# Kernel optimization log

Hardware: AMD Instinct MI355X
Metric: run time of the kernel (lower is better)

Reference implementation:

```python
import jax, jax.numpy as jnp
import numpy as np

NEG_SLOPE = 0.2


def _gat_layer(x, edge_index, W, a_src, a_dst, b):
    """PyG GATConv: linear -> per-edge attention logits -> segment softmax over
    destination -> scatter-add weighted messages. Self-loops added (PyG default)."""
    N = x.shape[0]
    heads, out = a_src.shape
    loops = jnp.arange(N, dtype=edge_index.dtype)
    src = jnp.concatenate([edge_index[0], loops])
    dst = jnp.concatenate([edge_index[1], loops])
    xh = (x @ W).reshape(N, heads, out)                      # [N,H,D]
    alpha_s = (xh * a_src).sum(-1)                           # [N,H]
    alpha_d = (xh * a_dst).sum(-1)                           # [N,H]
    e = jax.nn.leaky_relu(alpha_s[src] + alpha_d[dst], NEG_SLOPE)  # [E,H]
    emax = jax.ops.segment_max(e, dst, num_segments=N)       # [N,H]
    ex = jnp.exp(e - emax[dst])
    den = jax.ops.segment_sum(ex, dst, num_segments=N)
    att = ex / (den[dst] + 1e-16)                            # [E,H]
    msg = xh[src] * att[..., None]                           # [E,H,D]
    o = jax.ops.segment_sum(msg, dst, num_segments=N)        # [N,H,D]
    return o.reshape(N, heads * out) + b


def _single_source_gnn(h, edge_index, params):
    n_layers = len(params)
    for i, (W, a_s, a_d, b) in enumerate(params):
        h = _gat_layer(h, edge_index, W, a_s, a_d, b)
        if i < n_layers - 1:
            h = jax.nn.relu(h)
    return h


def setup_inputs() -> dict:
    key = jax.random.key(0)
    B, N, H, heads, deg = 4, 2000, 64, 4, 32
    E = N * deg
    ks = jax.random.split(key, 20)

    def mk_edge_index(k):
        e = jax.random.randint(k, (2, B, E), 0, N)
        off = (jnp.arange(B) * N)[None, :, None]
        return (e + off).reshape(2, B * E).astype(jnp.int32)

    inp = {
        "h0_flat": jax.random.normal(ks[0], (B * N, H), jnp.float32),
        "edge_index_s1": mk_edge_index(ks[1]),
        "edge_index_s2": mk_edge_index(ks[2]),
    }
    dims = [(H, H * heads), (H * heads, H * heads)]
    i = 3
    for s in ("s1", "s2"):
        for l, (din, dout) in enumerate(dims):
            inp[f"W_{s}_{l}"] = jax.random.normal(ks[i], (din, dout), jnp.float32) * 0.1; i += 1
            inp[f"a_src_{s}_{l}"] = jax.random.normal(ks[i], (heads, H), jnp.float32) * 0.1; i += 1
            inp[f"a_dst_{s}_{l}"] = jax.random.normal(ks[i], (heads, H), jnp.float32) * 0.1; i += 1
            inp[f"b_{s}_{l}"] = jnp.zeros((dout,), jnp.float32)
    inp["batch_size"] = B
    inp["num_stocks"] = N
    return inp


def reference(h0_flat, edge_index_s1, edge_index_s2,
              W_s1_0, a_src_s1_0, a_dst_s1_0, b_s1_0,
              W_s1_1, a_src_s1_1, a_dst_s1_1, b_s1_1,
              W_s2_0, a_src_s2_0, a_dst_s2_0, b_s2_0,
              W_s2_1, a_src_s2_1, a_dst_s2_1, b_s2_1,
              batch_size, num_stocks):
    p1 = [(W_s1_0, a_src_s1_0, a_dst_s1_0, b_s1_0),
          (W_s1_1, a_src_s1_1, a_dst_s1_1, b_s1_1)]
    p2 = [(W_s2_0, a_src_s2_0, a_dst_s2_0, b_s2_0),
          (W_s2_1, a_src_s2_1, a_dst_s2_1, b_s2_1)]
    h1 = _single_source_gnn(h0_flat, edge_index_s1, p1)
    h2 = _single_source_gnn(h0_flat, edge_index_s2, p2)
    # dict of per-source outputs in torch -> stacked [n_sources, B*N, H*heads]
    return jnp.stack([h1, h2])
```

## Files before the change

### kernel.cpp

```cpp
#include <hip/hip_runtime.h>
#include <hip/hip_fp16.h>


#define NEG_SLOPE 0.2f
#define ELLW 96
#define EPT 8

typedef _Float16 half8 __attribute__((ext_vector_type(8)));
typedef float floatx4 __attribute__((ext_vector_type(4)));

struct Args {
    const float* h0;
    const int *ei1, *ei2;
    const float *W10, *W11, *W20, *W21;
    const float *as10, *ad10, *b10, *as11, *ad11, *b11;
    const float *as20, *ad20, *b20, *as21, *ad21, *b21;
    _Float16 *Wt10, *Wt20, *Wt11, *Wt21;
    float *vaS1, *vaD1, *vaS2, *vaD2;
    _Float16 *h0h;
    int *cnt, *slots;
    _Float16 *agg1, *agg2;
    _Float16 *xh1, *xh2;
    float *alS1, *alD1, *alS2, *alD2;
    float *out0, *out1;
    int N, E1, E2, AB;
};


__global__ __launch_bounds__(64) void prep_kernel(Args a) {
    int z = blockIdx.z, y = blockIdx.y, c = blockIdx.x;
    int t = threadIdx.x;
    int flat = ((z * gridDim.y + y) * gridDim.x + c) * 64 + t;
    int GT = gridDim.x * gridDim.y * gridDim.z * 64;
    if (flat < 2 * a.N) a.cnt[flat] = 0;
    for (int i = flat; i < a.N * 64; i += GT)
        a.h0h[i] = (_Float16)a.h0[i];
    if (y == 0) {
        const float* W  = z ? a.W20  : a.W10;
        _Float16*    Wt = z ? a.Wt20 : a.Wt10;
        Wt[(size_t)c * 64 + t] = (_Float16)W[(size_t)t * 256 + c];
        if (c < 8) {
            int h = c & 3, sel = c >> 2;
            const float* av = sel ? (z ? a.ad20 : a.ad10)
                                  : (z ? a.as20 : a.as10);
            float* va = sel ? (z ? a.vaD2 : a.vaD1)
                            : (z ? a.vaS2 : a.vaS1);
            float acc = 0.f;
            for (int cc = 0; cc < 64; cc++)
                acc += W[(size_t)t * 256 + h * 64 + cc] * av[h * 64 + cc];
            va[h * 64 + t] = acc;
        }
    } else {
        int k = (y - 1) * 64 + t;
        const float* W  = z ? a.W21  : a.W11;
        _Float16*    Wt = z ? a.Wt21 : a.Wt11;
        Wt[(size_t)c * 256 + k] = (_Float16)W[(size_t)k * 256 + c];
    }
}


__global__ __launch_bounds__(256) void scat_al0_kernel(Args a) {
    int b = blockIdx.x;
    int tid = threadIdx.x;
    if (b < a.AB) {
        int g = b * 4 + (tid >> 6);
        if (g >= 2 * a.N) return;
        int L = tid & 63;
        int s = (g >= a.N) ? 1 : 0;
        int i = g - s * a.N;
        const float* vaS = s ? a.vaS2 : a.vaS1;
        const float* vaD = s ? a.vaD2 : a.vaD1;
        float* alS = s ? a.alS2 : a.alS1;
        float* alD = s ? a.alD2 : a.alD1;
        float x = a.h0[(size_t)i * 64 + L];
#pragma unroll
        for (int h = 0; h < 4; h++) {
            float sv = x * vaS[h * 64 + L];
            float dv = x * vaD[h * 64 + L];
#pragma unroll
            for (int off = 32; off >= 1; off >>= 1) {
                sv += __shfl_xor(sv, off);
                dv += __shfl_xor(dv, off);
            }
            if (L == 0) {
                alS[i * 4 + h] = sv;
                alD[i * 4 + h] = dv;
            }
        }
    } else {
        int sb = b - a.AB;
        int r = sb & 7;
        int chunk = sb >> 3;
        int cpx = (2 * a.N) >> 3;
        int glo = r * cpx, ghi = glo + cpx;
        int tot1 = a.E1 + a.N;
        int tot = tot1 + a.E2 + a.N;
        int base = chunk * (256 * EPT);
#pragma unroll
        for (int k = 0; k < EPT; k++) {
            int j = base + k * 256 + tid;
            if (j >= tot) break;
            int s, jj; const int* ei; int E;
            if (j < tot1) { s = 0; jj = j;        ei = a.ei1; E = a.E1; }
            else          { s = 1; jj = j - tot1; ei = a.ei2; E = a.E2; }
            int dst = (jj < E) ? ei[E + jj] : (jj - E);
            int gg = s * a.N + dst;
            if (gg < glo || gg >= ghi) continue;
            int src = (jj < E) ? ei[jj] : dst;
            int pos = atomicAdd(&a.cnt[gg], 1);
            if (pos < ELLW) a.slots[(size_t)gg * ELLW + pos] = src;
        }
    }
}


__global__ __launch_bounds__(256) void attn_agg_kernel(Args a) {
    __shared__ float2 pairs[4][8][10];
    int tid = threadIdx.x;
    int h = tid >> 6, L = tid & 63, st = L >> 3, lc = L & 7;
    int b = blockIdx.x;
    int cpx = (2 * a.N) >> 3;
    int g = (b & 7) * cpx + (b >> 3);
    int s = (g >= a.N) ? 1 : 0;
    int dst = g - s * a.N;
    const float* alS = s ? a.alS2 : a.alS1;
    const float* alD = s ? a.alD2 : a.alD1;
    _Float16*    agg = s ? a.agg2 : a.agg1;

    const int* slots = a.slots + (size_t)g * ELLW;
    int pre = slots[L];
    int nd = a.cnt[g];
    if (nd > ELLW) nd = ELLW;
    float ad = alD[dst * 4 + h];
    const char* xb = (const char*)a.h0h + lc * 16;

    float acc[8] = {};
    float pden = 0.f;

    for (int c = 0; c < nd; c += 64) {
        int n = nd - c; if (n > 64) n = 64;
        int off = 0; float p = 0.f;
        if (L < n) {
            int src = (c == 0) ? pre : slots[c + L];
            float t = alS[src * 4 + h] + ad;
            t = (t > 0.f) ? t : NEG_SLOPE * t;
            p = __expf(t);
            off = src * 128;
        }
        pden += p;
        pairs[h][L & 7][L >> 3] = make_float2(__int_as_float(off), p);
        int iters = (n + 7) >> 3;
        for (int ii = 0; ii < iters; ii += 4) {
            float4 twoA = *(const float4*)&pairs[h][st][ii];
            float4 twoB = *(const float4*)&pairs[h][st][ii + 2];
            int   o0 = __float_as_int(twoA.x); float w0 = twoA.y;
            int   o1i = __float_as_int(twoA.z); float w1 = twoA.w;
            int   o2i = __float_as_int(twoB.x); float w2 = twoB.y;
            int   o3i = __float_as_int(twoB.z); float w3 = twoB.w;
            float4 r0 = *(const float4*)(xb + o0);
            float4 r1 = *(const float4*)(xb + o1i);
            float4 r2 = *(const float4*)(xb + o2i);
            float4 r3 = *(const float4*)(xb + o3i);
            const __half2* q0 = (const __half2*)&r0;
            const __half2* q1 = (const __half2*)&r1;
            const __half2* q2 = (const __half2*)&r2;
            const __half2* q3 = (const __half2*)&r3;
#pragma unroll
            for (int k = 0; k < 4; k++) {
                acc[2 * k + 0] += (float)q0[k].x * w0;
                acc[2 * k + 1] += (float)q0[k].y * w0;
                acc[2 * k + 0] += (float)q1[k].x * w1;
                acc[2 * k + 1] += (float)q1[k].y * w1;
                acc[2 * k + 0] += (float)q2[k].x * w2;
                acc[2 * k + 1] += (float)q2[k].y * w2;
                acc[2 * k + 0] += (float)q3[k].x * w3;
                acc[2 * k + 1] += (float)q3[k].y * w3;
            }
        }
    }
#pragma unroll
    for (int k = 0; k < 8; k++) {
        acc[k] += __shfl_xor(acc[k], 8);
        acc[k] += __shfl_xor(acc[k], 16);
        acc[k] += __shfl_xor(acc[k], 32);
    }
#pragma unroll
    for (int o2_ = 32; o2_ >= 1; o2_ >>= 1) pden += __shfl_xor(pden, o2_);

    if (st == 0) {
        float d = 1.0f / (pden + 1e-16f);
        int col = h * 64 + lc * 8;
        half8 ov;
#pragma unroll
        for (int k = 0; k < 8; k++) ov[k] = (_Float16)(acc[k] * d);
        *(half8*)(agg + (size_t)dst * 256 + col) = ov;
    }
}


__global__ __launch_bounds__(256) void fusedgemm_kernel(Args a) {
    __shared__ _Float16 hT[32][264];
    int half_ = (a.N / 32);
    int b = blockIdx.x;
    int s = (b >= half_);
    int bx = b - s * half_;
    int row0 = bx * 32;

    const _Float16* agg = s ? a.agg2 : a.agg1;
    const _Float16* Wt0 = s ? a.Wt20 : a.Wt10;
    const _Float16* Wt1 = s ? a.Wt21 : a.Wt11;
    const float* bias0  = s ? a.b20  : a.b10;
    const float* a_s    = s ? a.as21 : a.as11;
    const float* a_d    = s ? a.ad21 : a.ad11;
    _Float16* xh = s ? a.xh2 : a.xh1;
    float* alS = s ? a.alS2 : a.alS1;
    float* alD = s ? a.alD2 : a.alD1;

    int tid  = threadIdx.x;
    int wave = tid >> 6;
    int lane = tid & 63;
    int lo = lane & 15, hi = lane >> 4;
    int c0 = wave * 64;

    {
        floatx4 acc[2][4] = {};
#pragma unroll
        for (int ks = 0; ks < 2; ks++) {
            half8 af[2], bf[4];
#pragma unroll
            for (int f = 0; f < 2; f++)
                af[f] = *(const half8*)(agg + (size_t)(row0 + f * 16 + lo) * 256
                                        + c0 + ks * 32 + hi * 8);
#pragma unroll
            for (int cf = 0; cf < 4; cf++)
                bf[cf] = *(const half8*)(Wt0 + (size_t)(c0 + cf * 16 + lo) * 64
                                         + ks * 32 + hi * 8);
#pragma unroll
            for (int f = 0; f < 2; f++)
#pragma unroll
                for (int cf = 0; cf < 4; cf++)
                    acc[f][cf] = __builtin_amdgcn_mfma_f32_16x16x32_f16(
                        af[f], bf[cf], acc[f][cf], 0, 0, 0);
        }
        float bb[4];
#pragma unroll
        for (int cf = 0; cf < 4; cf++) bb[cf] = bias0[c0 + cf * 16 + lo];
#pragma unroll
        for (int f = 0; f < 2; f++)
#pragma unroll
            for (int cf = 0; cf < 4; cf++)
#pragma unroll
                for (int r = 0; r < 4; r++) {
                    int row = f * 16 + hi * 4 + r;
                    float v = acc[f][cf][r] + bb[cf];
                    hT[row][c0 + cf * 16 + lo] = (_Float16)fmaxf(v, 0.f);
                }
    }
    __syncthreads();

    floatx4 acc[2][4] = {};
#pragma unroll
    for (int ks = 0; ks < 8; ks++) {
        half8 af[2], bf[4];
#pragma unroll
        for (int f = 0; f < 2; f++)
            af[f] = *(const half8*)&hT[f * 16 + lo][ks * 32 + hi * 8];
#pragma unroll
        for (int cf = 0; cf < 4; cf++)
            bf[cf] = *(const half8*)(Wt1 + (size_t)(c0 + cf * 16 + lo) * 256
                                     + ks * 32 + hi * 8);
#pragma unroll
        for (int f = 0; f < 2; f++)
#pragma unroll
            for (int cf = 0; cf < 4; cf++)
                acc[f][cf] = __builtin_amdgcn_mfma_f32_16x16x32_f16(
                    af[f], bf[cf], acc[f][cf], 0, 0, 0);
    }

    float asw[4], adw[4];
#pragma unroll
    for (int cf = 0; cf < 4; cf++) {
        asw[cf] = a_s[c0 + cf * 16 + lo];
        adw[cf] = a_d[c0 + cf * 16 + lo];
    }
#pragma unroll
    for (int f = 0; f < 2; f++) {
#pragma unroll
        for (int r = 0; r < 4; r++) {
            int row = row0 + f * 16 + hi * 4 + r;
            float v0 = acc[f][0][r], v1 = acc[f][1][r];
            float v2 = acc[f][2][r], v3 = acc[f][3][r];
            _Float16* xrow = &xh[(size_t)row * 256 + c0 + lo];
            xrow[0]  = (_Float16)v0;
            xrow[16] = (_Float16)v1;
            xrow[32] = (_Float16)v2;
            xrow[48] = (_Float16)v3;
            float s1 = v0 * asw[0] + v1 * asw[1] + v2 * asw[2] + v3 * asw[3];
            float s2 = v0 * adw[0] + v1 * adw[1] + v2 * adw[2] + v3 * adw[3];
#pragma unroll
            for (int off = 1; off < 16; off <<= 1) {
                s1 += __shfl_xor(s1, off);
                s2 += __shfl_xor(s2, off);
            }
            if (lo == 0) {
                alS[row * 4 + wave] = s1;
                alD[row * 4 + wave] = s2;
            }
        }
    }
}


__global__ __launch_bounds__(256) void attn1_kernel(Args a) {
    __shared__ float2 pairs[4][8][10];
    int tid = threadIdx.x;
    int h = tid >> 6, L = tid & 63, st = L >> 3, lc = L & 7;
    int b = blockIdx.x;
    int cpx = (2 * a.N) >> 3;
    int g = (b & 7) * cpx + (b >> 3);
    int s = (g >= a.N) ? 1 : 0;
    int dst = g - s * a.N;
    const _Float16* xh = s ? a.xh2  : a.xh1;
    const float* alS   = s ? a.alS2 : a.alS1;
    const float* alD   = s ? a.alD2 : a.alD1;
    const float* bias  = s ? a.b21  : a.b11;
    float* out         = s ? a.out1 : a.out0;

    const int* slots = a.slots + (size_t)g * ELLW;
    int pre = slots[L];
    int nd = a.cnt[g];
    if (nd > ELLW) nd = ELLW;
    float ad = alD[dst * 4 + h];
    const char* xb = (const char*)xh + h * 128 + lc * 16;

    float acc[8] = {};
    float pden = 0.f;

    for (int c = 0; c < nd; c += 64) {
        int n = nd - c; if (n > 64) n = 64;
        int off = 0; float p = 0.f;
        if (L < n) {
            int src = (c == 0) ? pre : slots[c + L];
            float t = alS[src * 4 + h] + ad;
            t = (t > 0.f) ? t : NEG_SLOPE * t;
            p = __expf(t);
            off = src * 512;
        }
        pden += p;
        pairs[h][L & 7][L >> 3] = make_float2(__int_as_float(off), p);
        int iters = (n + 7) >> 3;
        for (int ii = 0; ii < iters; ii += 4) {
            float4 twoA = *(const float4*)&pairs[h][st][ii];
            float4 twoB = *(const float4*)&pairs[h][st][ii + 2];
            int   o0 = __float_as_int(twoA.x); float w0 = twoA.y;
            int   o1i = __float_as_int(twoA.z); float w1 = twoA.w;
            int   o2i = __float_as_int(twoB.x); float w2 = twoB.y;
            int   o3i = __float_as_int(twoB.z); float w3 = twoB.w;
            float4 r0 = *(const float4*)(xb + o0);
            float4 r1 = *(const float4*)(xb + o1i);
            float4 r2 = *(const float4*)(xb + o2i);
            float4 r3 = *(const float4*)(xb + o3i);
            const __half2* q0 = (const __half2*)&r0;
            const __half2* q1 = (const __half2*)&r1;
            const __half2* q2 = (const __half2*)&r2;
            const __half2* q3 = (const __half2*)&r3;
#pragma unroll
            for (int k = 0; k < 4; k++) {
                acc[2 * k + 0] += (float)q0[k].x * w0;
                acc[2 * k + 1] += (float)q0[k].y * w0;
                acc[2 * k + 0] += (float)q1[k].x * w1;
                acc[2 * k + 1] += (float)q1[k].y * w1;
                acc[2 * k + 0] += (float)q2[k].x * w2;
                acc[2 * k + 1] += (float)q2[k].y * w2;
                acc[2 * k + 0] += (float)q3[k].x * w3;
                acc[2 * k + 1] += (float)q3[k].y * w3;
            }
        }
    }
#pragma unroll
    for (int k = 0; k < 8; k++) {
        acc[k] += __shfl_xor(acc[k], 8);
        acc[k] += __shfl_xor(acc[k], 16);
        acc[k] += __shfl_xor(acc[k], 32);
    }
#pragma unroll
    for (int o2_ = 32; o2_ >= 1; o2_ >>= 1) pden += __shfl_xor(pden, o2_);

    if (st == 0) {
        float d = 1.0f / (pden + 1e-16f);
        int col = h * 64 + lc * 8;
        float4 bA = *(const float4*)&bias[col];
        float4 bB = *(const float4*)&bias[col + 4];
        float4 oA, oB;
        oA.x = acc[0] * d + bA.x; oA.y = acc[1] * d + bA.y;
        oA.z = acc[2] * d + bA.z; oA.w = acc[3] * d + bA.w;
        oB.x = acc[4] * d + bB.x; oB.y = acc[5] * d + bB.y;
        oB.z = acc[6] * d + bB.z; oB.w = acc[7] * d + bB.w;
        *(float4*)&out[(size_t)dst * 256 + col] = oA;
        *(float4*)&out[(size_t)dst * 256 + col + 4] = oB;
    }
}


extern "C" void kernel_launch(void* const* d_in, const int* in_sizes, int n_in,
                              void* d_out, int out_size, void* d_ws, size_t ws_size,
                              hipStream_t stream) {
    const int N  = in_sizes[0] / 64;
    const int E1 = in_sizes[1] / 2;
    const int E2 = in_sizes[2] / 2;

    char* base = (char*)d_ws;
    size_t off = 0;
    auto carve = [&](size_t bytes) -> void* {
        void* p = base + off;
        off += (bytes + 255) & ~(size_t)255;
        return p;
    };
    int* cnt        = (int*)carve((size_t)2 * N * 4);
    int* slots      = (int*)carve((size_t)2 * N * ELLW * 4);
    _Float16* agg1  = (_Float16*)carve((size_t)N * 256 * 2);
    _Float16* agg2  = (_Float16*)carve((size_t)N * 256 * 2);
    _Float16* xh1   = (_Float16*)carve((size_t)N * 256 * 2);
    _Float16* xh2   = (_Float16*)carve((size_t)N * 256 * 2);
    float* alS1     = (float*)carve((size_t)N * 4 * 4);
    float* alD1     = (float*)carve((size_t)N * 4 * 4);
    float* alS2     = (float*)carve((size_t)N * 4 * 4);
    float* alD2     = (float*)carve((size_t)N * 4 * 4);
    _Float16* Wt10  = (_Float16*)carve((size_t)256 * 64 * 2);
    _Float16* Wt20  = (_Float16*)carve((size_t)256 * 64 * 2);
    _Float16* Wt11  = (_Float16*)carve((size_t)256 * 256 * 2);
    _Float16* Wt21  = (_Float16*)carve((size_t)256 * 256 * 2);
    float* vaS1     = (float*)carve((size_t)256 * 4);
    float* vaD1     = (float*)carve((size_t)256 * 4);
    float* vaS2     = (float*)carve((size_t)256 * 4);
    float* vaD2     = (float*)carve((size_t)256 * 4);
    _Float16* h0h   = (_Float16*)carve((size_t)N * 64 * 2);
    (void)ws_size; (void)n_in;

    Args a;
    a.h0 = (const float*)d_in[0];
    a.ei1 = (const int*)d_in[1];
    a.ei2 = (const int*)d_in[2];
    a.W10 = (const float*)d_in[3];  a.as10 = (const float*)d_in[4];
    a.ad10 = (const float*)d_in[5]; a.b10 = (const float*)d_in[6];
    a.W11 = (const float*)d_in[7];  a.as11 = (const float*)d_in[8];
    a.ad11 = (const float*)d_in[9]; a.b11 = (const float*)d_in[10];
    a.W20 = (const float*)d_in[11]; a.as20 = (const float*)d_in[12];
    a.ad20 = (const float*)d_in[13]; a.b20 = (const float*)d_in[14];
    a.W21 = (const float*)d_in[15]; a.as21 = (const float*)d_in[16];
    a.ad21 = (const float*)d_in[17]; a.b21 = (const float*)d_in[18];
    a.Wt10 = Wt10; a.Wt20 = Wt20; a.Wt11 = Wt11; a.Wt21 = Wt21;
    a.vaS1 = vaS1; a.vaD1 = vaD1; a.vaS2 = vaS2; a.vaD2 = vaD2;
    a.h0h = h0h;
    a.cnt = cnt; a.slots = slots;
    a.agg1 = agg1; a.agg2 = agg2;
    a.xh1 = xh1; a.xh2 = xh2;
    a.alS1 = alS1; a.alD1 = alD1; a.alS2 = alS2; a.alD2 = alD2;
    a.out0 = (float*)d_out; a.out1 = (float*)d_out + (size_t)N * 256;
    a.N = N; a.E1 = E1; a.E2 = E2;
    a.AB = (2 * N + 3) / 4;

    int tot = (E1 + N) + (E2 + N);
    int chunks = (tot + 256 * EPT - 1) / (256 * EPT);
    int scatterBlocks = chunks * 8;

    prep_kernel<<<dim3(256, 5, 2), 64, 0, stream>>>(a);
    scat_al0_kernel<<<a.AB + scatterBlocks, 256, 0, stream>>>(a);
    attn_agg_kernel<<<2 * N, 256, 0, stream>>>(a);
    fusedgemm_kernel<<<(N / 32) * 2, 256, 0, stream>>>(a);
    attn1_kernel<<<2 * N, 256, 0, stream>>>(a);
}
```

Before: 114.1 us.

## Fuse prep, alpha projection, and edge scatter into one launch

Merges the weight transpose/fp16 conversion, the layer-0 attention-logit computation and the ELL scatter into a single kernel, replacing the separate prep launch with a memset plus one launch. Each alpha block now recomputes the folded W·a vectors in shared memory and computes logits for 64 nodes from a shared h0 tile, which removes the dependency on a prior kernel. This saves a launch and the serialization between the prep and scatter stages. In exchange it adds redundant va recomputation in every alpha block, and it assumes 2N is divisible by 64 and that no 64-node block straddles the source boundary.

```diff
diff --git a/kernel.cpp b/kernel.cpp
--- a/kernel.cpp
+++ b/kernel.cpp
@@ -5,6 +5,7 @@
 #define NEG_SLOPE 0.2f
 #define ELLW 96
 #define EPT 8
+#define NB_PREP 512
 
 typedef _Float16 half8 __attribute__((ext_vector_type(8)));
 typedef float floatx4 __attribute__((ext_vector_type(4)));
@@ -16,7 +17,6 @@
     const float *as10, *ad10, *b10, *as11, *ad11, *b11;
     const float *as20, *ad20, *b20, *as21, *ad21, *b21;
     _Float16 *Wt10, *Wt20, *Wt11, *Wt21;
-    float *vaS1, *vaD1, *vaS2, *vaD2;
     _Float16 *h0h;
     int *cnt, *slots;
     _Float16 *agg1, *agg2;
@@ -27,72 +27,80 @@
 };
 
 
-__global__ __launch_bounds__(64) void prep_kernel(Args a) {
-    int z = blockIdx.z, y = blockIdx.y, c = blockIdx.x;
-    int t = threadIdx.x;
-    int flat = ((z * gridDim.y + y) * gridDim.x + c) * 64 + t;
-    int GT = gridDim.x * gridDim.y * gridDim.z * 64;
-    if (flat < 2 * a.N) a.cnt[flat] = 0;
-    for (int i = flat; i < a.N * 64; i += GT)
-        a.h0h[i] = (_Float16)a.h0[i];
-    if (y == 0) {
-        const float* W  = z ? a.W20  : a.W10;
-        _Float16*    Wt = z ? a.Wt20 : a.Wt10;
-        Wt[(size_t)c * 64 + t] = (_Float16)W[(size_t)t * 256 + c];
-        if (c < 8) {
-            int h = c & 3, sel = c >> 2;
-            const float* av = sel ? (z ? a.ad20 : a.ad10)
-                                  : (z ? a.as20 : a.as10);
-            float* va = sel ? (z ? a.vaD2 : a.vaD1)
-                            : (z ? a.vaS2 : a.vaS1);
-            float acc = 0.f;
-            for (int cc = 0; cc < 64; cc++)
-                acc += W[(size_t)t * 256 + h * 64 + cc] * av[h * 64 + cc];
-            va[h * 64 + t] = acc;
-        }
-    } else {
-        int k = (y - 1) * 64 + t;
-        const float* W  = z ? a.W21  : a.W11;
-        _Float16*    Wt = z ? a.Wt21 : a.Wt11;
-        Wt[(size_t)c * 256 + k] = (_Float16)W[(size_t)k * 256 + c];
-    }
-}
-
-
-__global__ __launch_bounds__(256) void scat_al0_kernel(Args a) {
+__global__ __launch_bounds__(256) void mega_prep_kernel(Args a) {
     int b = blockIdx.x;
     int tid = threadIdx.x;
-    if (b < a.AB) {
-        int g = b * 4 + (tid >> 6);
-        if (g >= 2 * a.N) return;
-        int L = tid & 63;
-        int s = (g >= a.N) ? 1 : 0;
-        int i = g - s * a.N;
-        const float* vaS = s ? a.vaS2 : a.vaS1;
-        const float* vaD = s ? a.vaD2 : a.vaD1;
+
+    if (b < NB_PREP) {
+        int flat = b * 256 + tid;
+        int GT = NB_PREP * 256;
+        int totA = 32768;
+        int totB = totA + 131072;
+        int totC = totB + a.N * 64;
+        for (int i = flat; i < totC; i += GT) {
+            if (i < totA) {
+                int s = i >> 14, rem = i & 16383;
+                int c = rem >> 6, k = rem & 63;
+                const float* W = s ? a.W20 : a.W10;
+                _Float16* Wt = s ? a.Wt20 : a.Wt10;
+                Wt[c * 64 + k] = (_Float16)W[k * 256 + c];
+            } else if (i < totB) {
+                int i2 = i - totA;
+                int s = i2 >> 16, rem = i2 & 65535;
+                int c = rem >> 8, k = rem & 255;
+                const float* W = s ? a.W21 : a.W11;
+                _Float16* Wt = s ? a.Wt21 : a.Wt11;
+                Wt[c * 256 + k] = (_Float16)W[k * 256 + c];
+            } else {
+                int i3 = i - totB;
+                a.h0h[i3] = (_Float16)a.h0[i3];
+            }
+        }
+    } else if (b < NB_PREP + a.AB) {
+        __shared__ float va[8][64];
+        __shared__ float h0s[64][64];
+        int ab = b - NB_PREP;
+        int g0 = ab * 64;
+        int s = (g0 >= a.N) ? 1 : 0;
+        int i0 = g0 - s * a.N;
+        const float* W0 = s ? a.W20 : a.W10;
+        const float* aS = s ? a.as20 : a.as10;
+        const float* aD = s ? a.ad20 : a.ad10;
         float* alS = s ? a.alS2 : a.alS1;
         float* alD = s ? a.alD2 : a.alD1;
-        float x = a.h0[(size_t)i * 64 + L];
-#pragma unroll
-        for (int h = 0; h < 4; h++) {
-            float sv = x * vaS[h * 64 + L];
-            float dv = x * vaD[h * 64 + L];
-#pragma unroll
-            for (int off = 32; off >= 1; off >>= 1) {
-                sv += __shfl_xor(sv, off);
-                dv += __shfl_xor(dv, off);
-            }
-            if (L == 0) {
-                alS[i * 4 + h] = sv;
-                alD[i * 4 + h] = dv;
-            }
-        }
+#pragma unroll
+        for (int o = 0; o < 2; o++) {
+            int out = o * 256 + tid;
+            int sel = out >> 8, rem = out & 255;
+            int h = rem >> 6, t = rem & 63;
+            const float* av = sel ? aD : aS;
+            float acc = 0.f;
+            const float* wrow = W0 + (size_t)t * 256 + h * 64;
+            const float* arow = av + h * 64;
+            for (int cc = 0; cc < 64; cc++) acc += wrow[cc] * arow[cc];
+            va[sel * 4 + h][t] = acc;
+        }
+#pragma unroll
+        for (int e = 0; e < 16; e++) {
+            int idx = e * 256 + tid;
+            h0s[idx >> 6][idx & 63] = a.h0[(size_t)(i0 + (idx >> 6)) * 64 + (idx & 63)];
+        }
+        __syncthreads();
+        int r = tid >> 2, h = tid & 3;
+        float sv = 0.f, dv = 0.f;
+        for (int k = 0; k < 64; k++) {
+            float x = h0s[r][k];
+            sv += x * va[h][k];
+            dv += x * va[4 + h][k];
+        }
+        alS[(i0 + r) * 4 + h] = sv;
+        alD[(i0 + r) * 4 + h] = dv;
     } else {
-        int sb = b - a.AB;
-        int r = sb & 7;
+        int sb = b - NB_PREP - a.AB;
+        int rr = sb & 7;
         int chunk = sb >> 3;
         int cpx = (2 * a.N) >> 3;
-        int glo = r * cpx, ghi = glo + cpx;
+        int glo = rr * cpx, ghi = glo + cpx;
         int tot1 = a.E1 + a.N;
         int tot = tot1 + a.E2 + a.N;
         int base = chunk * (256 * EPT);
@@ -430,10 +438,6 @@
     _Float16* Wt20  = (_Float16*)carve((size_t)256 * 64 * 2);
     _Float16* Wt11  = (_Float16*)carve((size_t)256 * 256 * 2);
     _Float16* Wt21  = (_Float16*)carve((size_t)256 * 256 * 2);
-    float* vaS1     = (float*)carve((size_t)256 * 4);
-    float* vaD1     = (float*)carve((size_t)256 * 4);
-    float* vaS2     = (float*)carve((size_t)256 * 4);
-    float* vaD2     = (float*)carve((size_t)256 * 4);
     _Float16* h0h   = (_Float16*)carve((size_t)N * 64 * 2);
     (void)ws_size; (void)n_in;
 
@@ -450,7 +454,6 @@
     a.W21 = (const float*)d_in[15]; a.as21 = (const float*)d_in[16];
     a.ad21 = (const float*)d_in[17]; a.b21 = (const float*)d_in[18];
     a.Wt10 = Wt10; a.Wt20 = Wt20; a.Wt11 = Wt11; a.Wt21 = Wt21;
-    a.vaS1 = vaS1; a.vaD1 = vaD1; a.vaS2 = vaS2; a.vaD2 = vaD2;
     a.h0h = h0h;
     a.cnt = cnt; a.slots = slots;
     a.agg1 = agg1; a.agg2 = agg2;
@@ -458,14 +461,14 @@
     a.alS1 = alS1; a.alD1 = alD1; a.alS2 = alS2; a.alD2 = alD2;
     a.out0 = (float*)d_out; a.out1 = (float*)d_out + (size_t)N * 256;
     a.N = N; a.E1 = E1; a.E2 = E2;
-    a.AB = (2 * N + 3) / 4;
+    a.AB = (2 * N) / 64;
 
     int tot = (E1 + N) + (E2 + N);
     int chunks = (tot + 256 * EPT - 1) / (256 * EPT);
     int scatterBlocks = chunks * 8;
 
-    prep_kernel<<<dim3(256, 5, 2), 64, 0, stream>>>(a);
-    scat_al0_kernel<<<a.AB + scatterBlocks, 256, 0, stream>>>(a);
+    hipMemsetAsync(cnt, 0, (size_t)2 * N * 4, stream);
+    mega_prep_kernel<<<NB_PREP + a.AB + scatterBlocks, 256, 0, stream>>>(a);
     attn_agg_kernel<<<2 * N, 256, 0, stream>>>(a);
     fusedgemm_kernel<<<(N / 32) * 2, 256, 0, stream>>>(a);
     attn1_kernel<<<2 * N, 256, 0, stream>>>(a);
```

After: 110.6 us, median of 2. -3.1%, faster.
